# Kernel optimization log

Hardware: AMD Instinct MI355X
Metric: run time of the kernel (lower is better)

Reference implementation:

```python
import jax, jax.numpy as jnp
import numpy as np

SCALE = 8
NUM_CLASSES = 15
IGNORE_THRES = 0.5
# anchors for scale=8 divided by scale
GRID_ANCHOR = jnp.array([[96.0 / 8, 230.0 / 8], [79.0 / 8, 186.0 / 8], [81.0 / 8, 133.0 / 8]], dtype=jnp.float32)  # [3,2]


def _bce_sum(p, t, mask):
    # torch BCELoss(reduction='sum') with log clamped at -100, restricted to mask
    lp = jnp.maximum(jnp.log(p), -100.0)
    ln = jnp.maximum(jnp.log(1.0 - p), -100.0)
    return jnp.sum(-(t * lp + (1.0 - t) * ln) * mask)


def setup_inputs() -> dict:
    key = jax.random.key(0)
    k1, k2, k3 = jax.random.split(key, 3)
    nB, nG = 128, 52
    x = jax.random.normal(k1, (nB, 3 * (NUM_CLASSES + 5), nG, nG), dtype=jnp.float32)
    boxes = jax.random.uniform(k2, (nB, 4), minval=0.1, maxval=0.6)  # cx,cy,w,h in (0,1)
    cls = jax.random.randint(k3, (nB, 1), 0, NUM_CLASSES).astype(jnp.float32)
    labels = jnp.concatenate([boxes, cls], axis=-1)  # [nB,5]
    return {"x": x, "labels": labels}


def reference(x, labels):
    nB, nG = x.shape[0], x.shape[2]
    pred = x.reshape(nB, 3, NUM_CLASSES + 5, nG, nG).transpose(0, 1, 3, 4, 2)  # [B,3,G,G,20]
    px = jax.nn.sigmoid(pred[..., 0])
    py = jax.nn.sigmoid(pred[..., 1])
    pw = pred[..., 2]
    ph = pred[..., 3]
    conf = jax.nn.sigmoid(pred[..., 4])
    cls = jax.nn.softmax(pred[..., 5:], axis=-1)
    pred_boxs = jnp.stack([px, py, pw, ph], axis=-1)  # [B,3,G,G,4]
    out = jnp.concatenate([
        pred_boxs.reshape(nB, -1, 4) * SCALE,
        conf.reshape(nB, -1, 1),
        cls.reshape(nB, -1, NUM_CLASSES),
    ], axis=-1)

    # ---- build_targets (vectorized; one target per image as in original loop) ----
    tb = labels[:, :4] * nG  # boxes in grid units [B,4]
    gx, gy, gw, gh = tb[:, 0], tb[:, 1], tb[:, 2], tb[:, 3]
    gi = gx.astype(jnp.int32)
    gj = gy.astype(jnp.int32)
    gcls = labels[:, 4].astype(jnp.int32)

    # wh-IoU anchors vs targets -> [3,B]
    aw, ah = GRID_ANCHOR[:, 0:1], GRID_ANCHOR[:, 1:2]
    inter_wh = jnp.minimum(aw, gw[None, :]) * jnp.minimum(ah, gh[None, :])
    ious = inter_wh / (aw * ah + 1e-16 + gw[None, :] * gh[None, :] - inter_wh)
    best_idx = jnp.argmax(ious, axis=0)  # [B]

    bidx = jnp.arange(nB)
    shape4 = (nB, 3, nG, nG)
    obj = jnp.zeros(shape4, jnp.float32).at[bidx, best_idx, gj, gi].set(1.0)

    noobj = jnp.ones(shape4, jnp.float32)
    arep = jnp.tile(jnp.arange(3), nB)
    brep = jnp.repeat(bidx, 3)
    jrep = jnp.repeat(gj, 3)
    irep = jnp.repeat(gi, 3)
    ign = (jnp.reshape(ious.T, (-1,)) > IGNORE_THRES).astype(jnp.float32)
    noobj = noobj.at[brep, arep, jrep, irep].mul(1.0 - ign)
    noobj = noobj.at[bidx, best_idx, gj, gi].set(0.0)

    gif = gi.astype(jnp.float32)
    gjf = gj.astype(jnp.float32)
    tx = jnp.zeros(shape4, jnp.float32).at[bidx, best_idx, gj, gi].set(gx - gif)
    ty = jnp.zeros(shape4, jnp.float32).at[bidx, best_idx, gj, gi].set(gy - gjf)
    tw = jnp.zeros(shape4, jnp.float32).at[bidx, best_idx, gj, gi].set(jnp.log(gw / GRID_ANCHOR[best_idx, 0] + 1e-16))
    th = jnp.zeros(shape4, jnp.float32).at[bidx, best_idx, gj, gi].set(jnp.log(gh / GRID_ANCHOR[best_idx, 1] + 1e-16))
    tcls = jnp.zeros(shape4 + (NUM_CLASSES,), jnp.float32).at[bidx, best_idx, gj, gi, gcls].set(1.0)

    # cls_mask: does argmax of predicted class at target cell match gt class
    pred_cls_at = cls[bidx, best_idx, gj, gi]  # [B,15]
    cls_hit = (jnp.argmax(pred_cls_at, axis=-1) == gcls).astype(jnp.float32)
    cls_mask = jnp.zeros(shape4, jnp.float32).at[bidx, best_idx, gj, gi].set(cls_hit)

    # iou between pred box at target cell and target box (cxcywh, +1 corner convention)
    pb = pred_boxs[bidx, best_idx, gj, gi]  # [B,4]
    b1x1, b1y1 = pb[:, 0] - pb[:, 2] / 2, pb[:, 1] - pb[:, 3] / 2
    b1x2, b1y2 = pb[:, 0] + pb[:, 2] / 2, pb[:, 1] + pb[:, 3] / 2
    b2x1, b2y1 = gx - gw / 2, gy - gh / 2
    b2x2, b2y2 = gx + gw / 2, gy + gh / 2
    iw = jnp.clip(jnp.minimum(b1x2, b2x2) - jnp.maximum(b1x1, b2x1) + 1, 0)
    ih = jnp.clip(jnp.minimum(b1y2, b2y2) - jnp.maximum(b1y1, b2y1) + 1, 0)
    inter = iw * ih
    a1 = (b1x2 - b1x1 + 1) * (b1y2 - b1y1 + 1)
    a2 = (b2x2 - b2x1 + 1) * (b2y2 - b2y1 + 1)
    iou_vec = inter / (a1 + a2 - inter + 1e-16)
    iou_scores = jnp.zeros(shape4, jnp.float32).at[bidx, best_idx, gj, gi].set(iou_vec)

    tconf = obj
    # ---- losses (boolean-mask indexing replaced by masked sums) ----
    loss_x = jnp.sum(jnp.abs(px - tx) * obj)
    loss_y = jnp.sum(jnp.abs(py - ty) * obj)
    loss_w = jnp.sum(jnp.abs(pw - tw) * obj)
    loss_h = jnp.sum(jnp.abs(ph - th) * obj)
    loss_conf = _bce_sum(conf, tconf, obj) + 100.0 * _bce_sum(conf, tconf, noobj)
    loss_cls = _bce_sum(cls, tcls, obj[..., None])
    loss = loss_x + loss_y + loss_w + loss_h + loss_conf + loss_cls
    return (loss, out)
```

## Files before the change

### kernel.cpp

```cpp
#include <hip/hip_runtime.h>
#include <math.h>

#define NB   128
#define NG   52
#define NGG  (NG*NG)
#define NA   3
#define NCLS 15
#define NCH  20
#define NQ   (NA*NGG)
#define TOTAL (NB*NQ)
#define BLK  256
#define NBLK (TOTAL/BLK)

#define REC_STRIDE 16
#define ACC_OFF (NB*REC_STRIDE)

__global__ void prep_kernel(const float* __restrict__ labels, float* __restrict__ ws) {
    int b = threadIdx.x;
    if (b == 0) ws[ACC_OFF] = 0.0f;
    if (b < NB) {
        float gx = labels[b*5+0] * (float)NG;
        float gy = labels[b*5+1] * (float)NG;
        float gw = labels[b*5+2] * (float)NG;
        float gh = labels[b*5+3] * (float)NG;
        int gcls = (int)labels[b*5+4];
        int gi = (int)gx, gj = (int)gy;
        const float aw[3] = {12.0f, 9.875f, 10.125f};
        const float ah[3] = {28.75f, 23.25f, 16.625f};
        float iou[3];
        #pragma unroll
        for (int a = 0; a < 3; a++) {
            float inter = fminf(aw[a], gw) * fminf(ah[a], gh);
            iou[a] = inter / (aw[a]*ah[a] + 1e-16f + gw*gh - inter);
        }
        int best = 0; float bv = iou[0];
        if (iou[1] > bv) { best = 1; bv = iou[1]; }
        if (iou[2] > bv) { best = 2; bv = iou[2]; }
        float* r = ws + b*REC_STRIDE;
        r[0]  = __int_as_float(best);
        r[1]  = __int_as_float(gi);
        r[2]  = __int_as_float(gj);
        r[3]  = __int_as_float(gcls);
        r[4]  = gx - (float)gi;
        r[5]  = gy - (float)gj;
        r[6]  = logf(gw / aw[best] + 1e-16f);
        r[7]  = logf(gh / ah[best] + 1e-16f);
        r[8]  = (iou[0] > 0.5f) ? 1.0f : 0.0f;
        r[9]  = (iou[1] > 0.5f) ? 1.0f : 0.0f;
        r[10] = (iou[2] > 0.5f) ? 1.0f : 0.0f;
    }
}

__global__ __launch_bounds__(BLK) void main_kernel(const float* __restrict__ x,
                                                   float* __restrict__ out,
                                                   float* __restrict__ acc) {
    int tid = threadIdx.x;
    int idx = blockIdx.x * BLK + tid;
    int b  = idx / NQ;
    int r  = idx - b * NQ;
    int a  = r / NGG;
    int ji = r - a * NGG;

    const float* xp = x + ((size_t)(b*60 + a*20)) * NGG + ji;
    float z[NCH];
    #pragma unroll
    for (int c = 0; c < NCH; c++) z[c] = xp[(size_t)c * NGG];

    float px   = 1.0f / (1.0f + expf(-z[0]));
    float py   = 1.0f / (1.0f + expf(-z[1]));
    float conf = 1.0f / (1.0f + expf(-z[4]));

    float m = z[5];
    #pragma unroll
    for (int c = 6; c < NCH; c++) m = fmaxf(m, z[c]);
    float e[NCLS]; float s = 0.0f;
    #pragma unroll
    for (int c = 0; c < NCLS; c++) { e[c] = expf(z[5+c] - m); s += e[c]; }
    float inv = 1.0f / s;

    float v[NCH];
    v[0] = px * 8.0f; v[1] = py * 8.0f; v[2] = z[2] * 8.0f; v[3] = z[3] * 8.0f;
    v[4] = conf;
    #pragma unroll
    for (int c = 0; c < NCLS; c++) v[5+c] = e[c] * inv;

    float term = -fmaxf(logf(1.0f - conf), -100.0f);

    __shared__ float sm[BLK * 21];
    #pragma unroll
    for (int c = 0; c < NCH; c++) sm[tid*21 + c] = v[c];

    float rs = term;
    #pragma unroll
    for (int off = 32; off > 0; off >>= 1) rs += __shfl_down(rs, off, 64);
    __shared__ float wsum[BLK/64];
    if ((tid & 63) == 0) wsum[tid >> 6] = rs;

    __syncthreads();

    size_t ob = 1 + (size_t)blockIdx.x * (BLK * NCH);
    int cell = tid / NCH, cc = tid - (tid / NCH) * NCH;
    #pragma unroll
    for (int k = 0; k < NCH; k++) {
        out[ob + (size_t)k*BLK + tid] = sm[cell*21 + cc];
        cc += 16; cell += 12;
        if (cc >= NCH) { cc -= NCH; cell++; }
    }

    if (tid == 0) atomicAdd(acc, wsum[0] + wsum[1] + wsum[2] + wsum[3]);
}

__global__ void finish_kernel(const float* __restrict__ ws, float* __restrict__ out) {
    int b = threadIdx.x;
    float partial = 0.0f;
    {
        const float* r = ws + b*REC_STRIDE;
        int best = __float_as_int(r[0]);
        int gi   = __float_as_int(r[1]);
        int gj   = __float_as_int(r[2]);
        int gcls = __float_as_int(r[3]);
        float txv = r[4], tyv = r[5], twv = r[6], thv = r[7];
        float ign[3] = { r[8], r[9], r[10] };
        float corr = 0.0f;
        #pragma unroll
        for (int a = 0; a < 3; a++) {
            int q = a*NGG + gj*NG + gi;
            const float* ob = out + 1 + ((size_t)b*NQ + q) * NCH;
            float conf = ob[4];
            bool isbest = (a == best);
            if (isbest || ign[a] > 0.5f) {
                corr += -fmaxf(logf(1.0f - conf), -100.0f);
            }
            if (isbest) {
                partial += -fmaxf(logf(conf), -100.0f);
                float px = ob[0]*0.125f, py = ob[1]*0.125f;
                float pw = ob[2]*0.125f, ph = ob[3]*0.125f;
                partial += fabsf(px - txv) + fabsf(py - tyv)
                         + fabsf(pw - twv) + fabsf(ph - thv);
                for (int c = 0; c < NCLS; c++) {
                    float p = ob[5 + c];
                    if (c == gcls) partial += -fmaxf(logf(p),        -100.0f);
                    else           partial += -fmaxf(logf(1.0f - p), -100.0f);
                }
            }
        }
        partial -= 100.0f * corr;
    }
    __shared__ float red[128];
    red[b] = partial;
    __syncthreads();
    for (int s2 = 64; s2 > 0; s2 >>= 1) {
        if (b < s2) red[b] += red[b + s2];
        __syncthreads();
    }
    if (b == 0) out[0] = red[0] + 100.0f * ws[ACC_OFF];
}

extern "C" void kernel_launch(void* const* d_in, const int* in_sizes, int n_in,
                              void* d_out, int out_size, void* d_ws, size_t ws_size,
                              hipStream_t stream) {
    const float* x      = (const float*)d_in[0];
    const float* labels = (const float*)d_in[1];
    float* out = (float*)d_out;
    float* ws  = (float*)d_ws;

    hipLaunchKernelGGL(prep_kernel,   dim3(1),    dim3(128), 0, stream, labels, ws);
    hipLaunchKernelGGL(main_kernel,   dim3(NBLK), dim3(BLK), 0, stream, x, out, ws + ACC_OFF);
    hipLaunchKernelGGL(finish_kernel, dim3(1),    dim3(128), 0, stream, ws, out);
}
```

Measured before the change: 177.4 us.

## Process two cells per thread with vectorized float2 loads and float4 stores

Each thread now handles two adjacent grid cells, loading inputs as float2 and writing the output tile through shared memory with aligned float4 stores; the shared layout is shifted by three floats so the output offset of one lines up to 16 bytes. The global atomic accumulation is replaced by per-block partials reduced in the finish kernel, and the prep kernel is folded into the finish kernel, saving one launch. The aim is fewer memory instructions, wider transactions and less launch and atomic overhead. It adds boundary fix-ups for the misaligned edge floats and more registers per thread.

```diff
diff --git a/kernel.cpp b/kernel.cpp
--- a/kernel.cpp
+++ b/kernel.cpp
@@ -1,24 +1,111 @@
 #include <hip/hip_runtime.h>
 #include <math.h>
 
-#define NB   128
-#define NG   52
-#define NGG  (NG*NG)
-#define NA   3
-#define NCLS 15
-#define NCH  20
-#define NQ   (NA*NGG)
-#define TOTAL (NB*NQ)
-#define BLK  256
-#define NBLK (TOTAL/BLK)
+#define NB    128
+#define NG    52
+#define NGG   2704
+#define NA    3
+#define NCLS  15
+#define NCH   20
+#define NQ    8112
+#define TOTAL 1038336
+#define BLK   256
+#define CPT   2
+#define CPB   (BLK*CPT)
+#define NBLK  (TOTAL/CPB)
+#define FPB   (CPB*NCH)
+#define NQUAD ((FPB-4)/4)
 
-#define REC_STRIDE 16
-#define ACC_OFF (NB*REC_STRIDE)
+__global__ __launch_bounds__(BLK) void main_kernel(const float* __restrict__ x,
+                                                   float* __restrict__ out,
+                                                   float* __restrict__ partials) {
+    __shared__ __align__(16) float sm[FPB];
+    __shared__ float wred[BLK/64];
 
-__global__ void prep_kernel(const float* __restrict__ labels, float* __restrict__ ws) {
-    int b = threadIdx.x;
-    if (b == 0) ws[ACC_OFF] = 0.0f;
-    if (b < NB) {
+    int t = threadIdx.x;
+    int g = blockIdx.x * BLK + t;
+    int cell0 = g * CPT;
+    int b  = cell0 / NQ;
+    int r  = cell0 - b * NQ;
+    int a  = r / NGG;
+    int ji = r - a * NGG;
+
+    const float2* __restrict__ xp =
+        (const float2*)(x + ((size_t)(b*60 + a*20)) * NGG) + (ji >> 1);
+
+    float za[NCH], zb[NCH];
+    #pragma unroll
+    for (int c = 0; c < NCH; c++) {
+        float2 zz = xp[c * (NGG/2)];
+        za[c] = zz.x; zb[c] = zz.y;
+    }
+
+    float tsum = 0.0f;
+    #pragma unroll
+    for (int i = 0; i < CPT; i++) {
+        const float* z = (i == 0) ? za : zb;
+        float v[NCH];
+        float conf = 1.0f / (1.0f + expf(-z[4]));
+        v[0] = 8.0f / (1.0f + expf(-z[0]));
+        v[1] = 8.0f / (1.0f + expf(-z[1]));
+        v[2] = 8.0f * z[2];
+        v[3] = 8.0f * z[3];
+        v[4] = conf;
+        float m = z[5];
+        #pragma unroll
+        for (int c = 6; c < NCH; c++) m = fmaxf(m, z[c]);
+        float s = 0.0f;
+        #pragma unroll
+        for (int c = 0; c < NCLS; c++) { v[5+c] = expf(z[5+c] - m); s += v[5+c]; }
+        float inv = 1.0f / s;
+        #pragma unroll
+        for (int c = 0; c < NCLS; c++) v[5+c] *= inv;
+
+        tsum += -fmaxf(logf(1.0f - conf), -100.0f);
+
+        int cl = (t * CPT + i);
+        int base = cl * NCH - 3;
+        #pragma unroll
+        for (int c = 0; c < NCH; c++) {
+            int L = base + c;
+            if (L < 0) L += FPB;
+            sm[L] = v[c];
+        }
+    }
+
+    #pragma unroll
+    for (int off = 32; off > 0; off >>= 1) tsum += __shfl_down(tsum, off, 64);
+    if ((t & 63) == 0) wred[t >> 6] = tsum;
+
+    __syncthreads();
+
+    size_t gbase = (size_t)blockIdx.x * FPB;
+    float4* __restrict__ op = (float4*)(out + gbase + 4);
+    const float4* __restrict__ sp = (const float4*)sm;
+    #pragma unroll
+    for (int k = 0; k < 10; k++) {
+        int q = k * BLK + t;
+        if (q < NQUAD) op[q] = sp[q];
+    }
+    if (t == 0) {
+        out[gbase + 1]    = sm[FPB - 3];
+        out[gbase + 2]    = sm[FPB - 2];
+        out[gbase + 3]    = sm[FPB - 1];
+        out[gbase + FPB]  = sm[FPB - 4];
+        partials[blockIdx.x] = wred[0] + wred[1] + wred[2] + wred[3];
+    }
+}
+
+__global__ void finish_kernel(const float* __restrict__ labels,
+                              const float* __restrict__ partials,
+                              float* __restrict__ out) {
+    int t = threadIdx.x;
+    float s = 0.0f;
+    for (int q = t; q < NBLK; q += 256) s += partials[q];
+
+    float corr_part = 0.0f;
+    if (t < NB) {
+        int b = t;
         float gx = labels[b*5+0] * (float)NG;
         float gy = labels[b*5+1] * (float)NG;
         float gw = labels[b*5+2] * (float)NG;
@@ -36,91 +123,11 @@
         int best = 0; float bv = iou[0];
         if (iou[1] > bv) { best = 1; bv = iou[1]; }
         if (iou[2] > bv) { best = 2; bv = iou[2]; }
-        float* r = ws + b*REC_STRIDE;
-        r[0]  = __int_as_float(best);
-        r[1]  = __int_as_float(gi);
-        r[2]  = __int_as_float(gj);
-        r[3]  = __int_as_float(gcls);
-        r[4]  = gx - (float)gi;
-        r[5]  = gy - (float)gj;
-        r[6]  = logf(gw / aw[best] + 1e-16f);
-        r[7]  = logf(gh / ah[best] + 1e-16f);
-        r[8]  = (iou[0] > 0.5f) ? 1.0f : 0.0f;
-        r[9]  = (iou[1] > 0.5f) ? 1.0f : 0.0f;
-        r[10] = (iou[2] > 0.5f) ? 1.0f : 0.0f;
-    }
-}
+        float txv = gx - (float)gi;
+        float tyv = gy - (float)gj;
+        float twv = logf(gw / aw[best] + 1e-16f);
+        float thv = logf(gh / ah[best] + 1e-16f);
 
-__global__ __launch_bounds__(BLK) void main_kernel(const float* __restrict__ x,
-                                                   float* __restrict__ out,
-                                                   float* __restrict__ acc) {
-    int tid = threadIdx.x;
-    int idx = blockIdx.x * BLK + tid;
-    int b  = idx / NQ;
-    int r  = idx - b * NQ;
-    int a  = r / NGG;
-    int ji = r - a * NGG;
-
-    const float* xp = x + ((size_t)(b*60 + a*20)) * NGG + ji;
-    float z[NCH];
-    #pragma unroll
-    for (int c = 0; c < NCH; c++) z[c] = xp[(size_t)c * NGG];
-
-    float px   = 1.0f / (1.0f + expf(-z[0]));
-    float py   = 1.0f / (1.0f + expf(-z[1]));
-    float conf = 1.0f / (1.0f + expf(-z[4]));
-
-    float m = z[5];
-    #pragma unroll
-    for (int c = 6; c < NCH; c++) m = fmaxf(m, z[c]);
-    float e[NCLS]; float s = 0.0f;
-    #pragma unroll
-    for (int c = 0; c < NCLS; c++) { e[c] = expf(z[5+c] - m); s += e[c]; }
-    float inv = 1.0f / s;
-
-    float v[NCH];
-    v[0] = px * 8.0f; v[1] = py * 8.0f; v[2] = z[2] * 8.0f; v[3] = z[3] * 8.0f;
-    v[4] = conf;
-    #pragma unroll
-    for (int c = 0; c < NCLS; c++) v[5+c] = e[c] * inv;
-
-    float term = -fmaxf(logf(1.0f - conf), -100.0f);
-
-    __shared__ float sm[BLK * 21];
-    #pragma unroll
-    for (int c = 0; c < NCH; c++) sm[tid*21 + c] = v[c];
-
-    float rs = term;
-    #pragma unroll
-    for (int off = 32; off > 0; off >>= 1) rs += __shfl_down(rs, off, 64);
-    __shared__ float wsum[BLK/64];
-    if ((tid & 63) == 0) wsum[tid >> 6] = rs;
-
-    __syncthreads();
-
-    size_t ob = 1 + (size_t)blockIdx.x * (BLK * NCH);
-    int cell = tid / NCH, cc = tid - (tid / NCH) * NCH;
-    #pragma unroll
-    for (int k = 0; k < NCH; k++) {
-        out[ob + (size_t)k*BLK + tid] = sm[cell*21 + cc];
-        cc += 16; cell += 12;
-        if (cc >= NCH) { cc -= NCH; cell++; }
-    }
-
-    if (tid == 0) atomicAdd(acc, wsum[0] + wsum[1] + wsum[2] + wsum[3]);
-}
-
-__global__ void finish_kernel(const float* __restrict__ ws, float* __restrict__ out) {
-    int b = threadIdx.x;
-    float partial = 0.0f;
-    {
-        const float* r = ws + b*REC_STRIDE;
-        int best = __float_as_int(r[0]);
-        int gi   = __float_as_int(r[1]);
-        int gj   = __float_as_int(r[2]);
-        int gcls = __float_as_int(r[3]);
-        float txv = r[4], tyv = r[5], twv = r[6], thv = r[7];
-        float ign[3] = { r[8], r[9], r[10] };
         float corr = 0.0f;
         #pragma unroll
         for (int a = 0; a < 3; a++) {
@@ -128,32 +135,33 @@
             const float* ob = out + 1 + ((size_t)b*NQ + q) * NCH;
             float conf = ob[4];
             bool isbest = (a == best);
-            if (isbest || ign[a] > 0.5f) {
+            if (isbest || iou[a] > 0.5f) {
                 corr += -fmaxf(logf(1.0f - conf), -100.0f);
             }
             if (isbest) {
-                partial += -fmaxf(logf(conf), -100.0f);
+                corr_part += -fmaxf(logf(conf), -100.0f);
                 float px = ob[0]*0.125f, py = ob[1]*0.125f;
                 float pw = ob[2]*0.125f, ph = ob[3]*0.125f;
-                partial += fabsf(px - txv) + fabsf(py - tyv)
-                         + fabsf(pw - twv) + fabsf(ph - thv);
+                corr_part += fabsf(px - txv) + fabsf(py - tyv)
+                           + fabsf(pw - twv) + fabsf(ph - thv);
                 for (int c = 0; c < NCLS; c++) {
                     float p = ob[5 + c];
-                    if (c == gcls) partial += -fmaxf(logf(p),        -100.0f);
-                    else           partial += -fmaxf(logf(1.0f - p), -100.0f);
+                    if (c == gcls) corr_part += -fmaxf(logf(p),        -100.0f);
+                    else           corr_part += -fmaxf(logf(1.0f - p), -100.0f);
                 }
             }
         }
-        partial -= 100.0f * corr;
+        corr_part -= 100.0f * corr;
     }
-    __shared__ float red[128];
-    red[b] = partial;
+
+    __shared__ float red[256];
+    red[t] = 100.0f * s + corr_part;
     __syncthreads();
-    for (int s2 = 64; s2 > 0; s2 >>= 1) {
-        if (b < s2) red[b] += red[b + s2];
+    for (int s2 = 128; s2 > 0; s2 >>= 1) {
+        if (t < s2) red[t] += red[t + s2];
         __syncthreads();
     }
-    if (b == 0) out[0] = red[0] + 100.0f * ws[ACC_OFF];
+    if (t == 0) out[0] = red[0];
 }
 
 extern "C" void kernel_launch(void* const* d_in, const int* in_sizes, int n_in,
@@ -164,7 +172,6 @@
     float* out = (float*)d_out;
     float* ws  = (float*)d_ws;
 
-    hipLaunchKernelGGL(prep_kernel,   dim3(1),    dim3(128), 0, stream, labels, ws);
-    hipLaunchKernelGGL(main_kernel,   dim3(NBLK), dim3(BLK), 0, stream, x, out, ws + ACC_OFF);
-    hipLaunchKernelGGL(finish_kernel, dim3(1),    dim3(128), 0, stream, ws, out);
+    hipLaunchKernelGGL(main_kernel,   dim3(NBLK), dim3(BLK), 0, stream, x, out, ws);
+    hipLaunchKernelGGL(finish_kernel, dim3(1),    dim3(256), 0, stream, labels, ws, out);
 }
```

Result: faster. 157.3 us (-11.3%).
